# Kernel optimization log

Measured on AMD Instinct MI355X. Metric: run time of the kernel, lower is better.

The kernel has to match this reference:

```python
import jax, jax.numpy as jnp
from jax import lax
import numpy as np

K = 3
PAD = (K - 1) // 2
EPS = 1e-5


def setup_inputs() -> dict:
    key = jax.random.key(0)
    k0, k1, k2, k3 = jax.random.split(key, 4)
    B, C, O, H, W = 8, 128, 128, 64, 64
    x = jax.random.normal(k0, (B, C, H, W), jnp.float32)
    bn_gamma = jnp.ones((C,), jnp.float32)
    bn_beta = jnp.zeros((C,), jnp.float32)
    bn_mean = jnp.zeros((C,), jnp.float32)
    bn_var = jnp.ones((C,), jnp.float32)
    # small offset-conv weights -> realistic sub-pixel offsets
    w_off = jax.random.normal(k1, (2 * K * K, C, K, K), jnp.float32) * 0.01
    b_off = jnp.zeros((2 * K * K,), jnp.float32)
    w_dconv = jax.random.normal(k2, (O, C, K, K), jnp.float32) * (1.0 / np.sqrt(C * K * K))
    b_dconv = jax.random.normal(k3, (O,), jnp.float32) * 0.01
    return dict(x=x, bn_gamma=bn_gamma, bn_beta=bn_beta, bn_mean=bn_mean,
                bn_var=bn_var, w_off=w_off, b_off=b_off,
                w_dconv=w_dconv, b_dconv=b_dconv)


def _conv2d(x, w, b):
    y = lax.conv_general_dilated(
        x, w, window_strides=(1, 1), padding=[(PAD, PAD), (PAD, PAD)],
        dimension_numbers=('NCHW', 'OIHW', 'NCHW'))
    return y + b[None, :, None, None]


def _deform_conv2d(x, offsets, w, b):
    # torchvision DeformConv2d semantics (deform_groups=1, groups=1, stride=1)
    B, C, H, W = x.shape
    KK = K * K
    off = offsets.reshape(B, KK, 2, H, W)  # (dy, dx) per kernel tap
    dy, dx = off[:, :, 0], off[:, :, 1]    # [B,KK,H,W]
    kh = (jnp.arange(KK) // K).astype(x.dtype)
    kw = (jnp.arange(KK) % K).astype(x.dtype)
    # sampling positions: p0 + pk - pad + offset
    py = dy + jnp.arange(H, dtype=x.dtype)[None, None, :, None] + (kh - PAD)[None, :, None, None]
    px = dx + jnp.arange(W, dtype=x.dtype)[None, None, None, :] + (kw - PAD)[None, :, None, None]
    y0 = jnp.floor(py)
    x0 = jnp.floor(px)
    wy = py - y0
    wx = px - x0
    y0i = y0.astype(jnp.int32)
    x0i = x0.astype(jnp.int32)
    xflat = x.reshape(B, C, H * W)

    def gather(yi, xi):
        valid = (yi >= 0) & (yi < H) & (xi >= 0) & (xi < W)
        idx = jnp.clip(yi, 0, H - 1) * W + jnp.clip(xi, 0, W - 1)  # [B,KK,H,W]
        vals = jax.vmap(lambda xf, ii: xf[:, ii])(xflat, idx)      # [B,C,KK,H,W]
        return vals * valid[:, None].astype(x.dtype)

    # bilinear sample with implicit zero padding outside the image
    v = (((1 - wy) * (1 - wx))[:, None] * gather(y0i, x0i)
         + ((1 - wy) * wx)[:, None] * gather(y0i, x0i + 1)
         + (wy * (1 - wx))[:, None] * gather(y0i + 1, x0i)
         + (wy * wx)[:, None] * gather(y0i + 1, x0i + 1))  # [B,C,KK,H,W]
    out = jnp.einsum('bckhw,ock->bohw', v, w.reshape(w.shape[0], C, KK))
    return out + b[None, :, None, None]


def reference(x, bn_gamma, bn_beta, bn_mean, bn_var, w_off, b_off, w_dconv, b_dconv):
    # BN (inference form) + ReLU
    inv = bn_gamma * lax.rsqrt(bn_var + EPS)
    h = jnp.maximum((x - bn_mean[None, :, None, None]) * inv[None, :, None, None]
                    + bn_beta[None, :, None, None], 0.0)
    offsets = _conv2d(h, w_off, b_off)          # [B, 2*K*K, H, W]
    return _deform_conv2d(h, offsets, w_dconv, b_dconv)
```

## Files before the change

kernel.cpp:

```cpp
#include <hip/hip_runtime.h>

#define CC 128
#define OO 128
#define HH 64
#define WW 64
#define HW (HH*WW)

typedef __attribute__((ext_vector_type(8))) __bf16 bf16x8;
typedef __attribute__((ext_vector_type(4))) __bf16 bf16x4;
typedef __attribute__((ext_vector_type(4))) float  f32x4;

__global__ __launch_bounds__(256) void prep(
    const float* __restrict__ x,
    const float* __restrict__ gamma, const float* __restrict__ beta,
    const float* __restrict__ mean,  const float* __restrict__ var,
    const float* __restrict__ w_dconv, const float* __restrict__ w_off,
    __bf16* __restrict__ h,
    __bf16* __restrict__ wt_swz,
    __bf16* __restrict__ woff_swz)
{
    __shared__ float inv_s[128], bb_s[128];
    __shared__ __bf16 tile[64 * 130];
    int blk = blockIdx.x;
    int tid = threadIdx.x;

    if (blk >= 512) {
        int idx = (blk - 512) * 256 + tid;
        if (idx < 147456) {
            int j    = idx & 7;
            int lane = (idx >> 3) & 63;
            int og   = (idx >> 9) & 7;
            int ks   = (idx >> 12) & 3;
            int kk   = idx >> 14;
            int o = og * 16 + (lane & 15);
            int c = ks * 32 + (lane >> 4) * 8 + j;
            wt_swz[idx] = (__bf16)w_dconv[(o * 128 + c) * 9 + kk];
        }
        if (idx < 36864) {
            int j    = idx & 7;
            int lane = (idx >> 3) & 63;
            int og   = (idx >> 9) & 1;
            int ks   = (idx >> 10) & 3;
            int kk   = idx >> 12;
            int o = og * 16 + (lane & 15);
            int c = ks * 32 + (lane >> 4) * 8 + j;
            float v = (o < 18) ? w_off[o * 1152 + c * 9 + kk] : 0.f;
            woff_swz[idx] = (__bf16)v;
        }
        return;
    }

    int b = blk & 7, y = blk >> 3;
    if (tid < 128) {
        float iv = gamma[tid] * rsqrtf(var[tid] + 1e-5f);
        inv_s[tid] = iv;
        bb_s[tid]  = beta[tid] - mean[tid] * iv;
    }
    __syncthreads();

    const float* xb = x + (size_t)b * CC * HW + (size_t)y * WW;
    #pragma unroll
    for (int i = 0; i < 8; ++i) {
        int idx = i * 256 + tid;
        int c = idx >> 4, x4 = idx & 15;
        float4 v = *(const float4*)(xb + (size_t)c * HW + x4 * 4);
        float iv = inv_s[c], bb = bb_s[c];
        tile[(x4 * 4 + 0) * 130 + c] = (__bf16)fmaxf(v.x * iv + bb, 0.f);
        tile[(x4 * 4 + 1) * 130 + c] = (__bf16)fmaxf(v.y * iv + bb, 0.f);
        tile[(x4 * 4 + 2) * 130 + c] = (__bf16)fmaxf(v.z * iv + bb, 0.f);
        tile[(x4 * 4 + 3) * 130 + c] = (__bf16)fmaxf(v.w * iv + bb, 0.f);
    }
    __syncthreads();

    __bf16* hb = h + ((size_t)b * HW + (size_t)y * WW) * CC;
    #pragma unroll
    for (int i = 0; i < 2; ++i) {
        int idx = i * 256 + tid;
        int xx = idx >> 3, c16 = idx & 7;
        const uint* src = (const uint*)&tile[xx * 130 + c16 * 16];
        uint r0 = src[0], r1 = src[1], r2 = src[2], r3 = src[3];
        uint r4 = src[4], r5 = src[5], r6 = src[6], r7 = src[7];
        uint* dst = (uint*)(hb + (size_t)xx * CC + c16 * 16);
        *(uint4*)dst       = (uint4){r0, r1, r2, r3};
        *(uint4*)(dst + 4) = (uint4){r4, r5, r6, r7};
    }
}

__global__ __launch_bounds__(512, 4) void fused_mfma(
    const __bf16* __restrict__ h,
    const __bf16* __restrict__ woff_swz,
    const float* __restrict__ b_off,
    const __bf16* __restrict__ wt_swz,
    const float* __restrict__ b_dconv,
    float* __restrict__ out)
{
    __shared__ float pw[576 * 4];
    __shared__ ushort pidx[576 * 4];
    __shared__ __align__(16) __bf16 vt[2][64 * 136];
    __shared__ float offs_lds[18 * 64];

    int blk = blockIdx.x;
    int b = blk & 7, y = blk >> 3;
    int tid = threadIdx.x;
    int lane = tid & 63;
    int wv  = __builtin_amdgcn_readfirstlane(tid >> 6);
    int l15 = lane & 15, quad = lane >> 4;

    const __bf16* hb = h + (size_t)b * HW * CC;

    {
        const bf16x8* w8 = (const bf16x8*)woff_swz;
        int ma = wv & 3;
        int oga = wv >> 2;

        f32x4 acc = (f32x4){0.f, 0.f, 0.f, 0.f};

        uint4 pa[2];
        {
            int yy = y - 1;
            bool yok = (yy >= 0);
            #pragma unroll
            for (int i = 0; i < 2; ++i) {
                int idx = i * 512 + tid;
                int xx = idx >> 4, c8 = idx & 15;
                int xs = xx - 1;
                pa[i] = (uint4){0u, 0u, 0u, 0u};
                if (yok && xs >= 0)
                    pa[i] = *(const uint4*)(hb + ((size_t)yy * WW + xs) * CC + c8 * 8);
            }
        }

        for (int kk = 0; kk < 9; ++kk) {
            int buf = kk & 1;
            #pragma unroll
            for (int i = 0; i < 2; ++i) {
                int idx = i * 512 + tid;
                int xx = idx >> 4, c8 = idx & 15;
                *(uint4*)&vt[buf][xx * 136 + c8 * 8] = pa[i];
            }
            if (kk < 8) {
                int k2 = kk + 1;
                int dy = k2 / 3 - 1, dx = k2 % 3 - 1;
                int yy = y + dy;
                bool yok = (yy >= 0) && (yy < HH);
                #pragma unroll
                for (int i = 0; i < 2; ++i) {
                    int idx = i * 512 + tid;
                    int xx = idx >> 4, c8 = idx & 15;
                    int xs = xx + dx;
                    pa[i] = (uint4){0u, 0u, 0u, 0u};
                    if (yok && xs >= 0 && xs < WW)
                        pa[i] = *(const uint4*)(hb + ((size_t)yy * WW + xs) * CC + c8 * 8);
                }
            }
            asm volatile("s_waitcnt lgkmcnt(0)" ::: "memory");
            __builtin_amdgcn_s_barrier();
            #pragma unroll
            for (int ks = 0; ks < 4; ++ks) {
                int kb = ks * 32 + quad * 8;
                bf16x8 a  = *(const bf16x8*)&vt[buf][(ma * 16 + l15) * 136 + kb];
                bf16x8 b0 = w8[((kk * 4 + ks) * 2 + oga) * 64 + lane];
                acc = __builtin_amdgcn_mfma_f32_16x16x32_bf16(a, b0, acc, 0, 0, 0);
            }
        }

        {
            int oc = oga * 16 + l15;
            if (oc < 18) {
                float bias = b_off[oc];
                #pragma unroll
                for (int r = 0; r < 4; ++r) {
                    int xx = ma * 16 + quad * 4 + r;
                    offs_lds[oc * 64 + xx] = acc[r] + bias;
                }
            }
        }
    }
    __syncthreads();

    for (int e = tid; e < 576; e += 512) {
        int kk = e >> 6, xx = e & 63;
        float dy = offs_lds[(2 * kk) * 64 + xx];
        float dx = offs_lds[(2 * kk + 1) * 64 + xx];
        float py = dy + (float)y + (float)(kk / 3 - 1);
        float px = dx + (float)xx + (float)(kk % 3 - 1);
        float fy = floorf(py), fx = floorf(px);
        int y0 = (int)fy, x0 = (int)fx;
        float wy = py - fy, wx = px - fx;
        int y1 = y0 + 1, x1 = x0 + 1;
        bool vy0 = (y0 >= 0) && (y0 < HH);
        bool vy1 = (y1 >= 0) && (y1 < HH);
        bool vx0 = (x0 >= 0) && (x0 < WW);
        bool vx1 = (x1 >= 0) && (x1 < WW);
        int yc0 = min(max(y0, 0), HH - 1), yc1 = min(max(y1, 0), HH - 1);
        int xc0 = min(max(x0, 0), WW - 1), xc1 = min(max(x1, 0), WW - 1);
        pw[e * 4 + 0] = (vy0 && vx0) ? (1.f - wy) * (1.f - wx) : 0.f;
        pw[e * 4 + 1] = (vy0 && vx1) ? (1.f - wy) * wx         : 0.f;
        pw[e * 4 + 2] = (vy1 && vx0) ? wy * (1.f - wx)         : 0.f;
        pw[e * 4 + 3] = (vy1 && vx1) ? wy * wx                 : 0.f;
        pidx[e * 4 + 0] = (ushort)(yc0 * WW + xc0);
        pidx[e * 4 + 1] = (ushort)(yc0 * WW + xc1);
        pidx[e * 4 + 2] = (ushort)(yc1 * WW + xc0);
        pidx[e * 4 + 3] = (ushort)(yc1 * WW + xc1);
    }
    __syncthreads();

    const bf16x8* w8 = (const bf16x8*)wt_swz;

    f32x4 acc[4];
    #pragma unroll
    for (int mt = 0; mt < 4; ++mt)
        acc[mt] = (f32x4){0.f, 0.f, 0.f, 0.f};

    bf16x8 pt0[2], pt1[2], pt2[2], pt3[2];
    #pragma unroll
    for (int i = 0; i < 2; ++i) {
        int idx = i * 512 + tid;
        int xx = idx >> 4, c8 = idx & 15;
        int e = xx;
        pt0[i] = *(const bf16x8*)(hb + ((int)pidx[e * 4 + 0] << 7) + c8 * 8);
        pt1[i] = *(const bf16x8*)(hb + ((int)pidx[e * 4 + 1] << 7) + c8 * 8);
        pt2[i] = *(const bf16x8*)(hb + ((int)pidx[e * 4 + 2] << 7) + c8 * 8);
        pt3[i] = *(const bf16x8*)(hb + ((int)pidx[e * 4 + 3] << 7) + c8 * 8);
    }

    for (int kk = 0; kk < 9; ++kk) {
        int buf = kk & 1;
        #pragma unroll
        for (int i = 0; i < 2; ++i) {
            int idx = i * 512 + tid;
            int xx = idx >> 4, c8 = idx & 15;
            int e = (kk << 6) + xx;
            float w0 = pw[e * 4 + 0], w1 = pw[e * 4 + 1];
            float w2 = pw[e * 4 + 2], w3 = pw[e * 4 + 3];
            bf16x8 pk;
            #pragma unroll
            for (int q = 0; q < 8; ++q) {
                float v = w0 * (float)pt0[i][q] + w1 * (float)pt1[i][q]
                        + w2 * (float)pt2[i][q] + w3 * (float)pt3[i][q];
                pk[q] = (__bf16)v;
            }
            *(bf16x8*)&vt[buf][xx * 136 + c8 * 8] = pk;
        }
        if (kk < 8) {
            #pragma unroll
            for (int i = 0; i < 2; ++i) {
                int idx = i * 512 + tid;
                int xx = idx >> 4, c8 = idx & 15;
                int e2 = ((kk + 1) << 6) + xx;
                pt0[i] = *(const bf16x8*)(hb + ((int)pidx[e2 * 4 + 0] << 7) + c8 * 8);
                pt1[i] = *(const bf16x8*)(hb + ((int)pidx[e2 * 4 + 1] << 7) + c8 * 8);
                pt2[i] = *(const bf16x8*)(hb + ((int)pidx[e2 * 4 + 2] << 7) + c8 * 8);
                pt3[i] = *(const bf16x8*)(hb + ((int)pidx[e2 * 4 + 3] << 7) + c8 * 8);
            }
        }
        asm volatile("s_waitcnt lgkmcnt(0)" ::: "memory");
        __builtin_amdgcn_s_barrier();
        #pragma unroll
        for (int ks = 0; ks < 4; ++ks) {
            int kb = ks * 32 + quad * 8;
            bf16x8 b0 = w8[((kk * 4 + ks) * 8 + wv) * 64 + lane];
            bf16x8 a0 = *(const bf16x8*)&vt[buf][(0 * 16 + l15) * 136 + kb];
            bf16x8 a1 = *(const bf16x8*)&vt[buf][(1 * 16 + l15) * 136 + kb];
            bf16x8 a2 = *(const bf16x8*)&vt[buf][(2 * 16 + l15) * 136 + kb];
            bf16x8 a3 = *(const bf16x8*)&vt[buf][(3 * 16 + l15) * 136 + kb];
            acc[0] = __builtin_amdgcn_mfma_f32_16x16x32_bf16(a0, b0, acc[0], 0, 0, 0);
            acc[1] = __builtin_amdgcn_mfma_f32_16x16x32_bf16(a1, b0, acc[1], 0, 0, 0);
            acc[2] = __builtin_amdgcn_mfma_f32_16x16x32_bf16(a2, b0, acc[2], 0, 0, 0);
            acc[3] = __builtin_amdgcn_mfma_f32_16x16x32_bf16(a3, b0, acc[3], 0, 0, 0);
        }
    }

    size_t ob = (size_t)b * OO * HW + (size_t)y * WW;
    {
        int o = wv * 16 + l15;
        float bias = b_dconv[o];
        #pragma unroll
        for (int mt = 0; mt < 4; ++mt) {
            int xb = mt * 16 + quad * 4;
            float4 r;
            r.x = acc[mt][0] + bias;
            r.y = acc[mt][1] + bias;
            r.z = acc[mt][2] + bias;
            r.w = acc[mt][3] + bias;
            *(float4*)&out[ob + (size_t)o * HW + xb] = r;
        }
    }
}

extern "C" void kernel_launch(void* const* d_in, const int* in_sizes, int n_in,
                              void* d_out, int out_size, void* d_ws, size_t ws_size,
                              hipStream_t stream)
{
    const float* x       = (const float*)d_in[0];
    const float* gamma   = (const float*)d_in[1];
    const float* beta    = (const float*)d_in[2];
    const float* mean    = (const float*)d_in[3];
    const float* var     = (const float*)d_in[4];
    const float* w_off   = (const float*)d_in[5];
    const float* b_off   = (const float*)d_in[6];
    const float* w_dconv = (const float*)d_in[7];
    const float* b_dconv = (const float*)d_in[8];
    float* out = (float*)d_out;

    char* ws = (char*)d_ws;
    __bf16* h_bf     = (__bf16*)ws;
    __bf16* wt_swz   = (__bf16*)(ws + 8388608);
    __bf16* woff_swz = (__bf16*)(ws + 8683520);

    prep<<<1232, 256, 0, stream>>>(x, gamma, beta, mean, var,
                                   w_dconv, w_off, h_bf, wt_swz, woff_swz);
    fused_mfma<<<512, 512, 0, stream>>>(h_bf, woff_swz, b_off,
                                        wt_swz, b_dconv, out);
}
```

Before: 117.7 us.

## Split each output row into two 32-pixel halves to double block count

The fused kernel now launches 1024 blocks instead of 512, each handling 32 pixels of a row rather than 64. LDS buffers and accumulators shrink accordingly, and the launch bounds ask for 6 blocks per CU instead of 4. The aim is more blocks in flight per CU on a 256-CU part, to hide gather and load latency. In exchange, dconv weight loads per output double and each MFMA weight fragment is reused half as often. Half the waves also now compute duplicate offset-conv results.

```diff
diff --git a/kernel.cpp b/kernel.cpp
--- a/kernel.cpp
+++ b/kernel.cpp
@@ -86,7 +86,7 @@
     }
 }
 
-__global__ __launch_bounds__(512, 4) void fused_mfma(
+__global__ __launch_bounds__(512, 6) void fused_mfma(
     const __bf16* __restrict__ h,
     const __bf16* __restrict__ woff_swz,
     const float* __restrict__ b_off,
@@ -94,64 +94,51 @@
     const float* __restrict__ b_dconv,
     float* __restrict__ out)
 {
-    __shared__ float pw[576 * 4];
-    __shared__ ushort pidx[576 * 4];
-    __shared__ __align__(16) __bf16 vt[2][64 * 136];
-    __shared__ float offs_lds[18 * 64];
+    __shared__ float pw[288 * 4];
+    __shared__ ushort pidx[288 * 4];
+    __shared__ __align__(16) __bf16 vt[2][32 * 136];
+    __shared__ float offs_lds[18 * 32];
 
     int blk = blockIdx.x;
-    int b = blk & 7, y = blk >> 3;
+    int b  = blk & 7;
+    int y  = (blk >> 3) & 63;
+    int x0 = (blk >> 9) * 32;
     int tid = threadIdx.x;
     int lane = tid & 63;
     int wv  = __builtin_amdgcn_readfirstlane(tid >> 6);
     int l15 = lane & 15, quad = lane >> 4;
 
+    int sxx = tid >> 4, sc8 = tid & 15;
+
     const __bf16* hb = h + (size_t)b * HW * CC;
 
     {
         const bf16x8* w8 = (const bf16x8*)woff_swz;
-        int ma = wv & 3;
-        int oga = wv >> 2;
+        int ma  = wv & 1;
+        int oga = (wv >> 1) & 1;
 
         f32x4 acc = (f32x4){0.f, 0.f, 0.f, 0.f};
 
-        uint4 pa[2];
+        uint4 pa;
         {
             int yy = y - 1;
-            bool yok = (yy >= 0);
-            #pragma unroll
-            for (int i = 0; i < 2; ++i) {
-                int idx = i * 512 + tid;
-                int xx = idx >> 4, c8 = idx & 15;
-                int xs = xx - 1;
-                pa[i] = (uint4){0u, 0u, 0u, 0u};
-                if (yok && xs >= 0)
-                    pa[i] = *(const uint4*)(hb + ((size_t)yy * WW + xs) * CC + c8 * 8);
-            }
+            int xs = x0 + sxx - 1;
+            pa = (uint4){0u, 0u, 0u, 0u};
+            if (yy >= 0 && xs >= 0 && xs < WW)
+                pa = *(const uint4*)(hb + ((size_t)yy * WW + xs) * CC + sc8 * 8);
         }
 
         for (int kk = 0; kk < 9; ++kk) {
             int buf = kk & 1;
-            #pragma unroll
-            for (int i = 0; i < 2; ++i) {
-                int idx = i * 512 + tid;
-                int xx = idx >> 4, c8 = idx & 15;
-                *(uint4*)&vt[buf][xx * 136 + c8 * 8] = pa[i];
-            }
+            *(uint4*)&vt[buf][sxx * 136 + sc8 * 8] = pa;
             if (kk < 8) {
                 int k2 = kk + 1;
                 int dy = k2 / 3 - 1, dx = k2 % 3 - 1;
                 int yy = y + dy;
-                bool yok = (yy >= 0) && (yy < HH);
-                #pragma unroll
-                for (int i = 0; i < 2; ++i) {
-                    int idx = i * 512 + tid;
-                    int xx = idx >> 4, c8 = idx & 15;
-                    int xs = xx + dx;
-                    pa[i] = (uint4){0u, 0u, 0u, 0u};
-                    if (yok && xs >= 0 && xs < WW)
-                        pa[i] = *(const uint4*)(hb + ((size_t)yy * WW + xs) * CC + c8 * 8);
-                }
+                int xs = x0 + sxx + dx;
+                pa = (uint4){0u, 0u, 0u, 0u};
+                if (yy >= 0 && yy < HH && xs >= 0 && xs < WW)
+                    pa = *(const uint4*)(hb + ((size_t)yy * WW + xs) * CC + sc8 * 8);
             }
             asm volatile("s_waitcnt lgkmcnt(0)" ::: "memory");
             __builtin_amdgcn_s_barrier();
@@ -170,30 +157,31 @@
                 float bias = b_off[oc];
                 #pragma unroll
                 for (int r = 0; r < 4; ++r) {
-                    int xx = ma * 16 + quad * 4 + r;
-                    offs_lds[oc * 64 + xx] = acc[r] + bias;
+                    int xxl = ma * 16 + quad * 4 + r;
+                    offs_lds[oc * 32 + xxl] = acc[r] + bias;
                 }
             }
         }
     }
     __syncthreads();
 
-    for (int e = tid; e < 576; e += 512) {
-        int kk = e >> 6, xx = e & 63;
-        float dy = offs_lds[(2 * kk) * 64 + xx];
-        float dx = offs_lds[(2 * kk + 1) * 64 + xx];
+    if (tid < 288) {
+        int e = tid;
+        int kk = e >> 5, xxl = e & 31;
+        float dy = offs_lds[(2 * kk) * 32 + xxl];
+        float dx = offs_lds[(2 * kk + 1) * 32 + xxl];
         float py = dy + (float)y + (float)(kk / 3 - 1);
-        float px = dx + (float)xx + (float)(kk % 3 - 1);
+        float px = dx + (float)(x0 + xxl) + (float)(kk % 3 - 1);
         float fy = floorf(py), fx = floorf(px);
-        int y0 = (int)fy, x0 = (int)fx;
+        int y0 = (int)fy, xq0 = (int)fx;
         float wy = py - fy, wx = px - fx;
-        int y1 = y0 + 1, x1 = x0 + 1;
+        int y1 = y0 + 1, xq1 = xq0 + 1;
         bool vy0 = (y0 >= 0) && (y0 < HH);
         bool vy1 = (y1 >= 0) && (y1 < HH);
-        bool vx0 = (x0 >= 0) && (x0 < WW);
-        bool vx1 = (x1 >= 0) && (x1 < WW);
+        bool vx0 = (xq0 >= 0) && (xq0 < WW);
+        bool vx1 = (xq1 >= 0) && (xq1 < WW);
         int yc0 = min(max(y0, 0), HH - 1), yc1 = min(max(y1, 0), HH - 1);
-        int xc0 = min(max(x0, 0), WW - 1), xc1 = min(max(x1, 0), WW - 1);
+        int xc0 = min(max(xq0, 0), WW - 1), xc1 = min(max(xq1, 0), WW - 1);
         pw[e * 4 + 0] = (vy0 && vx0) ? (1.f - wy) * (1.f - wx) : 0.f;
         pw[e * 4 + 1] = (vy0 && vx1) ? (1.f - wy) * wx         : 0.f;
         pw[e * 4 + 2] = (vy1 && vx0) ? wy * (1.f - wx)         : 0.f;
@@ -207,52 +195,40 @@
 
     const bf16x8* w8 = (const bf16x8*)wt_swz;
 
-    f32x4 acc[4];
-    #pragma unroll
-    for (int mt = 0; mt < 4; ++mt)
-        acc[mt] = (f32x4){0.f, 0.f, 0.f, 0.f};
-
-    bf16x8 pt0[2], pt1[2], pt2[2], pt3[2];
-    #pragma unroll
-    for (int i = 0; i < 2; ++i) {
-        int idx = i * 512 + tid;
-        int xx = idx >> 4, c8 = idx & 15;
-        int e = xx;
-        pt0[i] = *(const bf16x8*)(hb + ((int)pidx[e * 4 + 0] << 7) + c8 * 8);
-        pt1[i] = *(const bf16x8*)(hb + ((int)pidx[e * 4 + 1] << 7) + c8 * 8);
-        pt2[i] = *(const bf16x8*)(hb + ((int)pidx[e * 4 + 2] << 7) + c8 * 8);
-        pt3[i] = *(const bf16x8*)(hb + ((int)pidx[e * 4 + 3] << 7) + c8 * 8);
+    f32x4 acc[2];
+    acc[0] = (f32x4){0.f, 0.f, 0.f, 0.f};
+    acc[1] = (f32x4){0.f, 0.f, 0.f, 0.f};
+
+    bf16x8 pt0, pt1, pt2, pt3;
+    {
+        int e = sxx;
+        pt0 = *(const bf16x8*)(hb + ((int)pidx[e * 4 + 0] << 7) + sc8 * 8);
+        pt1 = *(const bf16x8*)(hb + ((int)pidx[e * 4 + 1] << 7) + sc8 * 8);
+        pt2 = *(const bf16x8*)(hb + ((int)pidx[e * 4 + 2] << 7) + sc8 * 8);
+        pt3 = *(const bf16x8*)(hb + ((int)pidx[e * 4 + 3] << 7) + sc8 * 8);
     }
 
     for (int kk = 0; kk < 9; ++kk) {
         int buf = kk & 1;
-        #pragma unroll
-        for (int i = 0; i < 2; ++i) {
-            int idx = i * 512 + tid;
-            int xx = idx >> 4, c8 = idx & 15;
-            int e = (kk << 6) + xx;
+        {
+            int e = (kk << 5) + sxx;
             float w0 = pw[e * 4 + 0], w1 = pw[e * 4 + 1];
             float w2 = pw[e * 4 + 2], w3 = pw[e * 4 + 3];
             bf16x8 pk;
             #pragma unroll
             for (int q = 0; q < 8; ++q) {
-                float v = w0 * (float)pt0[i][q] + w1 * (float)pt1[i][q]
-                        + w2 * (float)pt2[i][q] + w3 * (float)pt3[i][q];
+                float v = w0 * (float)pt0[q] + w1 * (float)pt1[q]
+                        + w2 * (float)pt2[q] + w3 * (float)pt3[q];
                 pk[q] = (__bf16)v;
             }
-            *(bf16x8*)&vt[buf][xx * 136 + c8 * 8] = pk;
+            *(bf16x8*)&vt[buf][sxx * 136 + sc8 * 8] = pk;
         }
         if (kk < 8) {
-            #pragma unroll
-            for (int i = 0; i < 2; ++i) {
-                int idx = i * 512 + tid;
-                int xx = idx >> 4, c8 = idx & 15;
-                int e2 = ((kk + 1) << 6) + xx;
-                pt0[i] = *(const bf16x8*)(hb + ((int)pidx[e2 * 4 + 0] << 7) + c8 * 8);
-                pt1[i] = *(const bf16x8*)(hb + ((int)pidx[e2 * 4 + 1] << 7) + c8 * 8);
-                pt2[i] = *(const bf16x8*)(hb + ((int)pidx[e2 * 4 + 2] << 7) + c8 * 8);
-                pt3[i] = *(const bf16x8*)(hb + ((int)pidx[e2 * 4 + 3] << 7) + c8 * 8);
-            }
+            int e2 = ((kk + 1) << 5) + sxx;
+            pt0 = *(const bf16x8*)(hb + ((int)pidx[e2 * 4 + 0] << 7) + sc8 * 8);
+            pt1 = *(const bf16x8*)(hb + ((int)pidx[e2 * 4 + 1] << 7) + sc8 * 8);
+            pt2 = *(const bf16x8*)(hb + ((int)pidx[e2 * 4 + 2] << 7) + sc8 * 8);
+            pt3 = *(const bf16x8*)(hb + ((int)pidx[e2 * 4 + 3] << 7) + sc8 * 8);
         }
         asm volatile("s_waitcnt lgkmcnt(0)" ::: "memory");
         __builtin_amdgcn_s_barrier();
@@ -262,12 +238,8 @@
             bf16x8 b0 = w8[((kk * 4 + ks) * 8 + wv) * 64 + lane];
             bf16x8 a0 = *(const bf16x8*)&vt[buf][(0 * 16 + l15) * 136 + kb];
             bf16x8 a1 = *(const bf16x8*)&vt[buf][(1 * 16 + l15) * 136 + kb];
-            bf16x8 a2 = *(const bf16x8*)&vt[buf][(2 * 16 + l15) * 136 + kb];
-            bf16x8 a3 = *(const bf16x8*)&vt[buf][(3 * 16 + l15) * 136 + kb];
             acc[0] = __builtin_amdgcn_mfma_f32_16x16x32_bf16(a0, b0, acc[0], 0, 0, 0);
             acc[1] = __builtin_amdgcn_mfma_f32_16x16x32_bf16(a1, b0, acc[1], 0, 0, 0);
-            acc[2] = __builtin_amdgcn_mfma_f32_16x16x32_bf16(a2, b0, acc[2], 0, 0, 0);
-            acc[3] = __builtin_amdgcn_mfma_f32_16x16x32_bf16(a3, b0, acc[3], 0, 0, 0);
         }
     }
 
@@ -276,8 +248,8 @@
         int o = wv * 16 + l15;
         float bias = b_dconv[o];
         #pragma unroll
-        for (int mt = 0; mt < 4; ++mt) {
-            int xb = mt * 16 + quad * 4;
+        for (int mt = 0; mt < 2; ++mt) {
+            int xb = x0 + mt * 16 + quad * 4;
             float4 r;
             r.x = acc[mt][0] + bias;
             r.y = acc[mt][1] + bias;
@@ -310,6 +282,6 @@
 
     prep<<<1232, 256, 0, stream>>>(x, gamma, beta, mean, var,
                                    w_dconv, w_off, h_bf, wt_swz, woff_swz);
-    fused_mfma<<<512, 512, 0, stream>>>(h_bf, woff_swz, b_off,
-                                        wt_swz, b_dconv, out);
+    fused_mfma<<<1024, 512, 0, stream>>>(h_bf, woff_swz, b_off,
+                                         wt_swz, b_dconv, out);
 }
```

Result: slower. 120.5 us (+2.4%).

## Stage 3-row halo tile once for offset conv instead of per-tap reloads

Applied to the files above, without the earlier changes.

The offset convolution now loads the three input rows (with zero-padded halo columns) into shared memory once, then indexes shifted windows for all nine taps. This replaces nine global reload/store/barrier rounds with a single load and one sync. Shared memory is reorganized into one aliased byte buffer so the larger tile reuses the space of the later-stage arrays, though total LDS use grows, which may lower occupancy.

```diff
diff --git a/kernel.cpp b/kernel.cpp
--- a/kernel.cpp
+++ b/kernel.cpp
@@ -94,10 +94,12 @@
     const float* __restrict__ b_dconv,
     float* __restrict__ out)
 {
-    __shared__ float pw[576 * 4];
-    __shared__ ushort pidx[576 * 4];
-    __shared__ __align__(16) __bf16 vt[2][64 * 136];
-    __shared__ float offs_lds[18 * 64];
+    __shared__ __align__(16) char smem[58464];
+    __bf16* tile3    = (__bf16*)smem;
+    float*  offs_lds = (float*)(smem + 53856);
+    float*  pw   = (float*)smem;
+    ushort* pidx = (ushort*)(smem + 9216);
+    __bf16* vt   = (__bf16*)(smem + 13824);
 
     int blk = blockIdx.x;
     int b = blk & 7, y = blk >> 3;
@@ -109,56 +111,39 @@
     const __bf16* hb = h + (size_t)b * HW * CC;
 
     {
+        if (tid < 96) {
+            int r = tid >> 5, col = (tid >> 4) & 1, c8 = tid & 15;
+            *(uint4*)&tile3[((r * 66) + (col ? 65 : 0)) * 136 + c8 * 8] =
+                (uint4){0u, 0u, 0u, 0u};
+        }
+        #pragma unroll
+        for (int i = 0; i < 6; ++i) {
+            int s  = i * 512 + tid;
+            int r  = s >> 10;
+            int xx = (s >> 4) & 63;
+            int c8 = s & 15;
+            int yy = y + r - 1;
+            uint4 v = (uint4){0u, 0u, 0u, 0u};
+            if (yy >= 0 && yy < HH)
+                v = *(const uint4*)(hb + ((size_t)yy * WW + xx) * CC + c8 * 8);
+            *(uint4*)&tile3[(r * 66 + xx + 1) * 136 + c8 * 8] = v;
+        }
+        __syncthreads();
+
         const bf16x8* w8 = (const bf16x8*)woff_swz;
-        int ma = wv & 3;
+        int ma  = wv & 3;
         int oga = wv >> 2;
 
         f32x4 acc = (f32x4){0.f, 0.f, 0.f, 0.f};
-
-        uint4 pa[2];
-        {
-            int yy = y - 1;
-            bool yok = (yy >= 0);
-            #pragma unroll
-            for (int i = 0; i < 2; ++i) {
-                int idx = i * 512 + tid;
-                int xx = idx >> 4, c8 = idx & 15;
-                int xs = xx - 1;
-                pa[i] = (uint4){0u, 0u, 0u, 0u};
-                if (yok && xs >= 0)
-                    pa[i] = *(const uint4*)(hb + ((size_t)yy * WW + xs) * CC + c8 * 8);
-            }
-        }
-
+        #pragma unroll
         for (int kk = 0; kk < 9; ++kk) {
-            int buf = kk & 1;
-            #pragma unroll
-            for (int i = 0; i < 2; ++i) {
-                int idx = i * 512 + tid;
-                int xx = idx >> 4, c8 = idx & 15;
-                *(uint4*)&vt[buf][xx * 136 + c8 * 8] = pa[i];
-            }
-            if (kk < 8) {
-                int k2 = kk + 1;
-                int dy = k2 / 3 - 1, dx = k2 % 3 - 1;
-                int yy = y + dy;
-                bool yok = (yy >= 0) && (yy < HH);
-                #pragma unroll
-                for (int i = 0; i < 2; ++i) {
-                    int idx = i * 512 + tid;
-                    int xx = idx >> 4, c8 = idx & 15;
-                    int xs = xx + dx;
-                    pa[i] = (uint4){0u, 0u, 0u, 0u};
-                    if (yok && xs >= 0 && xs < WW)
-                        pa[i] = *(const uint4*)(hb + ((size_t)yy * WW + xs) * CC + c8 * 8);
-                }
-            }
-            asm volatile("s_waitcnt lgkmcnt(0)" ::: "memory");
-            __builtin_amdgcn_s_barrier();
+            int dyi = kk / 3, dx = kk % 3 - 1;
+            const __bf16* arow =
+                &tile3[(dyi * 66 + ma * 16 + l15 + dx + 1) * 136];
             #pragma unroll
             for (int ks = 0; ks < 4; ++ks) {
                 int kb = ks * 32 + quad * 8;
-                bf16x8 a  = *(const bf16x8*)&vt[buf][(ma * 16 + l15) * 136 + kb];
+                bf16x8 a  = *(const bf16x8*)&arow[kb];
                 bf16x8 b0 = w8[((kk * 4 + ks) * 2 + oga) * 64 + lane];
                 acc = __builtin_amdgcn_mfma_f32_16x16x32_bf16(a, b0, acc, 0, 0, 0);
             }
@@ -225,7 +210,7 @@
     }
 
     for (int kk = 0; kk < 9; ++kk) {
-        int buf = kk & 1;
+        __bf16* vtb = vt + (kk & 1) * 8704;
         #pragma unroll
         for (int i = 0; i < 2; ++i) {
             int idx = i * 512 + tid;
@@ -240,7 +225,7 @@
                         + w2 * (float)pt2[i][q] + w3 * (float)pt3[i][q];
                 pk[q] = (__bf16)v;
             }
-            *(bf16x8*)&vt[buf][xx * 136 + c8 * 8] = pk;
+            *(bf16x8*)&vtb[xx * 136 + c8 * 8] = pk;
         }
         if (kk < 8) {
             #pragma unroll
@@ -260,10 +245,10 @@
         for (int ks = 0; ks < 4; ++ks) {
             int kb = ks * 32 + quad * 8;
             bf16x8 b0 = w8[((kk * 4 + ks) * 8 + wv) * 64 + lane];
-            bf16x8 a0 = *(const bf16x8*)&vt[buf][(0 * 16 + l15) * 136 + kb];
-            bf16x8 a1 = *(const bf16x8*)&vt[buf][(1 * 16 + l15) * 136 + kb];
-            bf16x8 a2 = *(const bf16x8*)&vt[buf][(2 * 16 + l15) * 136 + kb];
-            bf16x8 a3 = *(const bf16x8*)&vt[buf][(3 * 16 + l15) * 136 + kb];
+            bf16x8 a0 = *(const bf16x8*)&vtb[(0 * 16 + l15) * 136 + kb];
+            bf16x8 a1 = *(const bf16x8*)&vtb[(1 * 16 + l15) * 136 + kb];
+            bf16x8 a2 = *(const bf16x8*)&vtb[(2 * 16 + l15) * 136 + kb];
+            bf16x8 a3 = *(const bf16x8*)&vtb[(3 * 16 + l15) * 136 + kb];
             acc[0] = __builtin_amdgcn_mfma_f32_16x16x32_bf16(a0, b0, acc[0], 0, 0, 0);
             acc[1] = __builtin_amdgcn_mfma_f32_16x16x32_bf16(a1, b0, acc[1], 0, 0, 0);
             acc[2] = __builtin_amdgcn_mfma_f32_16x16x32_bf16(a2, b0, acc[2], 0, 0, 0);
```

Result: no change. 116.0 us (-1.4%).
